# Performance work log

Measured on AMD Instinct MI355X. Metric: run time of the kernel, lower is better.

The kernel has to match this reference:

```python
import jax, jax.numpy as jnp
import numpy as np

KERNEL = 3
STRIDE = 1
PADDING = 1


def _extract_patches(x, k, stride, padding, h_out, w_out):
    # x: [B, C, H, W] -> patches [k, k, B, C, h_out, w_out]
    if padding > 0:
        x = jnp.pad(x, ((0, 0), (0, 0), (padding, padding), (padding, padding)))
    rows = []
    for di in range(k):
        cols = []
        for dj in range(k):
            sl = x[:, :, di:di + (h_out - 1) * stride + 1:stride,
                        dj:dj + (w_out - 1) * stride + 1:stride]
            cols.append(sl)
        rows.append(jnp.stack(cols, axis=0))
    return jnp.stack(rows, axis=0)  # [k, k, B, C, h_out, w_out]


def setup_inputs() -> dict:
    key = jax.random.key(0)
    k1, k2 = jax.random.split(key)
    B, C_in, C_out, H, W = 32, 64, 64, 32, 32
    h_out = (H + 2 * PADDING - KERNEL) // STRIDE + 1
    w_out = (W + 2 * PADDING - KERNEL) // STRIDE + 1
    fan_in = C_in * KERNEL ** 2
    x = jax.random.normal(k1, (B, C_in, H, W), dtype=jnp.float32)
    weight = jax.random.normal(
        k2, (h_out, w_out, C_out, C_in, KERNEL, KERNEL), dtype=jnp.float32
    ) / np.sqrt(fan_in).astype(np.float32)
    bias = jnp.zeros((C_out, h_out, w_out), dtype=jnp.float32)
    return {"x": x, "weight": weight, "bias": bias}


def reference(x, weight, bias):
    h_out, w_out = weight.shape[0], weight.shape[1]
    # patches: [k, k, B, C, h_out, w_out]
    patches = _extract_patches(x, KERNEL, STRIDE, PADDING, h_out, w_out)
    # unshared-weight contraction per spatial location
    # weight: [h_out(x), w_out(y), O, C(i), k(k), k(l)]
    out = jnp.einsum('xyoikl,klbixy->boxy', weight, patches)
    return out + bias[None, :, :, :]
```

## Files before the change

kernel.cpp:

```cpp
#include <hip/hip_runtime.h>

#define CIN 64
#define COUT 64
#define BATCH 32
#define KTOT 576
#define NPOS 1024

__device__ float g_xT[CIN * 34 * 34 * BATCH];

__global__ __launch_bounds__(256) void repack_kernel(const float* __restrict__ x) {
    __shared__ float tile[32 * 33];
    const int i   = blockIdx.x;
    const int hh  = blockIdx.y;
    const int tid = threadIdx.x;

    float* dst = &g_xT[((i * 34 + hh) * 34) * BATCH];

    if (hh == 0 || hh == 33) {
        for (int idx = tid; idx < 34 * BATCH; idx += 256) dst[idx] = 0.f;
        return;
    }
    const int hs = hh - 1;
#pragma unroll
    for (int bb = 0; bb < 4; ++bb) {
        int b = bb * 8 + (tid >> 5);
        int w = tid & 31;
        tile[b * 33 + w] = x[(b << 16) + (i << 10) + (hs << 5) + w];
    }
    __syncthreads();
#pragma unroll
    for (int q = 0; q < 5; ++q) {
        int ww = q * 8 + (tid >> 5);
        if (ww < 34) {
            int b = tid & 31;
            float v = (ww == 0 || ww == 33) ? 0.f : tile[b * 33 + (ww - 1)];
            dst[ww * BATCH + b] = v;
        }
    }
}

__global__ __launch_bounds__(512, 4) void local2d_kernel(
    const float* __restrict__ weight,
    const float* __restrict__ bias,
    float* __restrict__ out)
{
    __shared__ __align__(16) float lds[144 * 32 * 4];

    const int tid = threadIdx.x;
    const int wv  = tid >> 6;
    const int l   = tid & 63;
    const int bg  = l & 7;
    const int og2 = l >> 3;

    int bid = blockIdx.x;
    int xcd = bid & 7;
    int t   = bid >> 3;
    int oh  = t & 1;
    int tt  = t >> 1;
    int y   = ((tt >> 5) << 3) | xcd;
    int xw  = tt & 31;
    int p   = (y << 5) | xw;

    {
        const float* src = weight + ((long)p * COUT + (oh << 5)) * KTOT
                         + (tid & 31) * KTOT + ((tid >> 5) << 2);
#pragma unroll
        for (int q = 0; q < 9; ++q) {
            *(float4*)(&lds[((q << 9) + tid) << 2]) =
                *(const float4*)(src + (q << 6));
        }
    }
    __syncthreads();

    float acc[4][4];
#pragma unroll
    for (int a = 0; a < 4; ++a)
#pragma unroll
        for (int c = 0; c < 4; ++c) acc[a][c] = 0.f;

    const float* pb = g_xT + (((wv << 3) * 1156 + y * 34 + xw) << 5) + (bg << 2);
    const float* wb = &lds[(wv * 2304) + (og2 << 2)];

#pragma unroll
    for (int g = 0; g < 18; ++g) {
        float4 pr[4];
#pragma unroll
        for (int j = 0; j < 4; ++j) {
            const int c  = 4 * g + j;
            const int di = c / 9;
            const int rr = c - 9 * di;
            const int kh = rr / 3;
            const int kw = rr - 3 * kh;
            pr[j] = *(const float4*)(pb + ((di * 1156 + kh * 34 + kw) << 5));
        }
        const float* prf = (const float*)pr;
#pragma unroll
        for (int oc = 0; oc < 4; ++oc) {
            float4 wr = *(const float4*)(wb + (g << 7) + (oc << 5));
#pragma unroll
            for (int bb = 0; bb < 4; ++bb) {
                float a = acc[oc][bb];
                a = fmaf(wr.x, prf[0 * 4 + bb], a);
                a = fmaf(wr.y, prf[1 * 4 + bb], a);
                a = fmaf(wr.z, prf[2 * 4 + bb], a);
                a = fmaf(wr.w, prf[3 * 4 + bb], a);
                acc[oc][bb] = a;
            }
        }
    }

    __syncthreads();
    if (wv != 0) {
        float* R = &lds[(wv - 1) * 1152];
#pragma unroll
        for (int oc = 0; oc < 4; ++oc) {
            int o = (oc << 3) + og2;
            *(float4*)(&R[o * 36 + (bg << 2)]) =
                make_float4(acc[oc][0], acc[oc][1], acc[oc][2], acc[oc][3]);
        }
    }
    __syncthreads();
    if (wv == 0) {
#pragma unroll
        for (int oc = 0; oc < 4; ++oc) {
            int o  = (oc << 3) + og2;
            int of = (oh << 5) + o;
            float s0 = acc[oc][0], s1 = acc[oc][1], s2 = acc[oc][2], s3 = acc[oc][3];
#pragma unroll
            for (int s = 0; s < 7; ++s) {
                float4 r = *(const float4*)(&lds[s * 1152 + o * 36 + (bg << 2)]);
                s0 += r.x; s1 += r.y; s2 += r.z; s3 += r.w;
            }
            float bv = bias[(of << 10) + p];
            int b0 = bg << 2;
            out[((b0 + 0) << 16) + (of << 10) + p] = s0 + bv;
            out[((b0 + 1) << 16) + (of << 10) + p] = s1 + bv;
            out[((b0 + 2) << 16) + (of << 10) + p] = s2 + bv;
            out[((b0 + 3) << 16) + (of << 10) + p] = s3 + bv;
        }
    }
}

extern "C" void kernel_launch(void* const* d_in, const int* in_sizes, int n_in,
                              void* d_out, int out_size, void* d_ws, size_t ws_size,
                              hipStream_t stream) {
    const float* x      = (const float*)d_in[0];
    const float* weight = (const float*)d_in[1];
    const float* bias   = (const float*)d_in[2];
    float* out          = (float*)d_out;

    hipLaunchKernelGGL(repack_kernel, dim3(CIN, 34), dim3(256), 0, stream, x);
    hipLaunchKernelGGL(local2d_kernel, dim3(2 * NPOS), dim3(512), 0, stream,
                       weight, bias, out);
}
```

Baseline: 262.7 us.

## Stage input patches in LDS and stream weights directly from global

Swaps which operand is staged in shared memory. The 576x32 patch tile is gathered from the repacked input into LDS, and the per-position weights, which are used only once, are read straight from global memory as float4 per thread. The block shrinks to 256 threads (4 waves), each wave covering 144 of the K dimension, which cuts the cross-wave reduction from 8 partials to 4. The cost is less latency hiding per block and uncoalesced strided global weight loads (each lane reads a different output row), in exchange for fewer LDS round trips on the weight stream.

Measured after the change: 319.0 us. +21.4%, slower.

```diff
diff --git a/kernel.cpp b/kernel.cpp
--- a/kernel.cpp
+++ b/kernel.cpp
@@ -5,6 +5,7 @@
 #define BATCH 32
 #define KTOT 576
 #define NPOS 1024
+#define KQ 144
 
 __device__ float g_xT[CIN * 34 * 34 * BATCH];
 
@@ -39,18 +40,18 @@
     }
 }
 
-__global__ __launch_bounds__(512, 4) void local2d_kernel(
+__global__ __launch_bounds__(256, 2) void local2d_kernel(
     const float* __restrict__ weight,
     const float* __restrict__ bias,
     float* __restrict__ out)
 {
-    __shared__ __align__(16) float lds[144 * 32 * 4];
+    __shared__ __align__(16) float Pl[4 * KQ * 32];
 
     const int tid = threadIdx.x;
     const int wv  = tid >> 6;
     const int l   = tid & 63;
-    const int bg  = l & 7;
-    const int og2 = l >> 3;
+    const int og  = l & 7;
+    const int bg  = l >> 3;
 
     int bid = blockIdx.x;
     int xcd = bid & 7;
@@ -61,16 +62,24 @@
     int xw  = tt & 31;
     int p   = (y << 5) | xw;
 
-    {
-        const float* src = weight + ((long)p * COUT + (oh << 5)) * KTOT
-                         + (tid & 31) * KTOT + ((tid >> 5) << 2);
-#pragma unroll
-        for (int q = 0; q < 9; ++q) {
-            *(float4*)(&lds[((q << 9) + tid) << 2]) =
-                *(const float4*)(src + (q << 6));
-        }
+    for (int q = 0; q < 18; ++q) {
+        int k  = (q << 5) + (tid >> 3);
+        int i  = k / 9;
+        int r  = k - i * 9;
+        int kh = r / 3;
+        int kw = r - kh * 3;
+        const float* ps =
+            &g_xT[((((i * 34) + y + kh) * 34 + xw + kw) << 5) + ((tid & 7) << 2)];
+        *(float4*)(&Pl[((q << 8) + tid) << 2]) = *(const float4*)ps;
     }
     __syncthreads();
+
+    const int kbase = wv * KQ;
+    const float* w0 = weight + ((long)p * COUT + (oh << 5) + 0  + og) * KTOT + kbase;
+    const float* w1 = w0 + 8 * KTOT;
+    const float* w2 = w0 + 16 * KTOT;
+    const float* w3 = w0 + 24 * KTOT;
+    const float* pb = Pl + wv * (KQ * 32) + (bg << 2);
 
     float acc[4][4];
 #pragma unroll
@@ -78,43 +87,41 @@
 #pragma unroll
         for (int c = 0; c < 4; ++c) acc[a][c] = 0.f;
 
-    const float* pb = g_xT + (((wv << 3) * 1156 + y * 34 + xw) << 5) + (bg << 2);
-    const float* wb = &lds[(wv * 2304) + (og2 << 2)];
-
+    for (int u = 0; u < 3; ++u) {
 #pragma unroll
-    for (int g = 0; g < 18; ++g) {
-        float4 pr[4];
+        for (int s = 0; s < 12; ++s) {
+            float4 pr[4];
 #pragma unroll
-        for (int j = 0; j < 4; ++j) {
-            const int c  = 4 * g + j;
-            const int di = c / 9;
-            const int rr = c - 9 * di;
-            const int kh = rr / 3;
-            const int kw = rr - 3 * kh;
-            pr[j] = *(const float4*)(pb + ((di * 1156 + kh * 34 + kw) << 5));
+            for (int j = 0; j < 4; ++j)
+                pr[j] = *(const float4*)(pb + (((s << 2) + j) << 5));
+            float4 wq[4];
+            wq[0] = *(const float4*)(w0 + (s << 2));
+            wq[1] = *(const float4*)(w1 + (s << 2));
+            wq[2] = *(const float4*)(w2 + (s << 2));
+            wq[3] = *(const float4*)(w3 + (s << 2));
+            const float* prf = (const float*)pr;
+#pragma unroll
+            for (int oc = 0; oc < 4; ++oc)
+#pragma unroll
+                for (int bb = 0; bb < 4; ++bb) {
+                    float a = acc[oc][bb];
+                    a = fmaf(wq[oc].x, prf[0 + bb],  a);
+                    a = fmaf(wq[oc].y, prf[4 + bb],  a);
+                    a = fmaf(wq[oc].z, prf[8 + bb],  a);
+                    a = fmaf(wq[oc].w, prf[12 + bb], a);
+                    acc[oc][bb] = a;
+                }
         }
-        const float* prf = (const float*)pr;
-#pragma unroll
-        for (int oc = 0; oc < 4; ++oc) {
-            float4 wr = *(const float4*)(wb + (g << 7) + (oc << 5));
-#pragma unroll
-            for (int bb = 0; bb < 4; ++bb) {
-                float a = acc[oc][bb];
-                a = fmaf(wr.x, prf[0 * 4 + bb], a);
-                a = fmaf(wr.y, prf[1 * 4 + bb], a);
-                a = fmaf(wr.z, prf[2 * 4 + bb], a);
-                a = fmaf(wr.w, prf[3 * 4 + bb], a);
-                acc[oc][bb] = a;
-            }
-        }
+        w0 += 48; w1 += 48; w2 += 48; w3 += 48;
+        pb += 48 * 32;
     }
 
     __syncthreads();
     if (wv != 0) {
-        float* R = &lds[(wv - 1) * 1152];
+        float* R = &Pl[(wv - 1) * 1152];
 #pragma unroll
         for (int oc = 0; oc < 4; ++oc) {
-            int o = (oc << 3) + og2;
+            int o = (oc << 3) + og;
             *(float4*)(&R[o * 36 + (bg << 2)]) =
                 make_float4(acc[oc][0], acc[oc][1], acc[oc][2], acc[oc][3]);
         }
@@ -123,12 +130,12 @@
     if (wv == 0) {
 #pragma unroll
         for (int oc = 0; oc < 4; ++oc) {
-            int o  = (oc << 3) + og2;
+            int o  = (oc << 3) + og;
             int of = (oh << 5) + o;
             float s0 = acc[oc][0], s1 = acc[oc][1], s2 = acc[oc][2], s3 = acc[oc][3];
 #pragma unroll
-            for (int s = 0; s < 7; ++s) {
-                float4 r = *(const float4*)(&lds[s * 1152 + o * 36 + (bg << 2)]);
+            for (int s = 0; s < 3; ++s) {
+                float4 r = *(const float4*)(&Pl[s * 1152 + o * 36 + (bg << 2)]);
                 s0 += r.x; s1 += r.y; s2 += r.z; s3 += r.w;
             }
             float bv = bias[(of << 10) + p];
@@ -150,6 +157,6 @@
     float* out          = (float*)d_out;
 
     hipLaunchKernelGGL(repack_kernel, dim3(CIN, 34), dim3(256), 0, stream, x);
-    hipLaunchKernelGGL(local2d_kernel, dim3(2 * NPOS), dim3(512), 0, stream,
+    hipLaunchKernelGGL(local2d_kernel, dim3(2 * NPOS), dim3(256), 0, stream,
                        weight, bias, out);
 }
```
